# Kernel optimization log

Hardware: AMD Instinct MI355X
Metric: run time of the kernel (lower is better)

The kernel has to match this reference:

```python
import jax, jax.numpy as jnp
import numpy as np

DN = ('NCHW', 'OIHW', 'NCHW')

def _conv(x, w, pad):
    return jax.lax.conv_general_dilated(x, w, window_strides=(1, 1),
                                        padding=[(pad, pad), (pad, pad)],
                                        dimension_numbers=DN)

def _channel_shuffle(x, perm):
    # x: [B, C, H, W]; perm: [C, H*W] per-channel spatial permutation
    B, C, H, W = x.shape
    y = jnp.take_along_axis(x.reshape(B, C, H * W), perm[None, :, :], axis=2)
    return y.reshape(B, C, H, W)

def setup_inputs() -> dict:
    key = jax.random.key(0)
    k = jax.random.split(key, 6)
    B, Cin, H, W = 32, 1024, 28, 28
    P1, P2, P3 = 256, 256, 1024
    HW = H * W
    x = jax.random.normal(k[0], (B, Cin, H, W), dtype=jnp.float32)
    w1 = jax.random.normal(k[1], (P1, Cin, 1, 1), dtype=jnp.float32) * np.sqrt(2.0 / Cin)
    wd = jax.random.normal(k[2], (P2, P1, 3, 3), dtype=jnp.float32) * np.sqrt(2.0 / (P1 * 9))
    w3 = jax.random.normal(k[3], (P3, P2, 1, 1), dtype=jnp.float32) * np.sqrt(2.0 / P2)
    perm_dconv = jax.vmap(lambda kk: jax.random.permutation(kk, HW))(
        jax.random.split(k[4], P1)).astype(jnp.int32)
    perm_res = jax.vmap(lambda kk: jax.random.permutation(kk, HW))(
        jax.random.split(k[5], Cin)).astype(jnp.int32)
    return {"x": x, "w1": w1, "wd": wd, "w3": w3,
            "perm_dconv": perm_dconv, "perm_res": perm_res}

def reference(x, w1, wd, w3, perm_dconv, perm_res):
    # conv1 (1x1) + relu
    y = jax.nn.relu(_conv(x, w1, 0))
    # Dconv_shuffle: per-channel spatial shuffle then 3x3 conv (pad=1), relu
    y = _channel_shuffle(y, perm_dconv)
    y = jax.nn.relu(_conv(y, wd, 1))
    # conv3 (1x1)
    y = _conv(y, w3, 0)
    # residual: per-channel spatially shuffled input, add, relu
    res = _channel_shuffle(x, perm_res)
    return jax.nn.relu(y + res)
```

## Files before the change

### kernel.cpp

```cpp
#include <hip/hip_runtime.h>
#include <hip/hip_bf16.h>

#define BATCH 32
#define CIN   1024
#define HW    784
#define WIMG  28
#define PADW  30
#define PADHW 900
#define P1    256
#define P2    256
#define P3    1024
#define NFLAT (BATCH * HW)

typedef __attribute__((ext_vector_type(8))) short bfrag_t;
typedef __attribute__((ext_vector_type(8))) unsigned short usvec8;
typedef __attribute__((ext_vector_type(4))) unsigned short usvec4;
typedef __attribute__((ext_vector_type(4))) float accvec_t;

static __device__ __forceinline__ unsigned short f2bf(float f) {
    union { __hip_bfloat16 h; unsigned short u; } cv;
    cv.h = __float2bfloat16(f);
    return cv.u;
}
static __device__ __forceinline__ float bf2f(unsigned short u) {
    union { float f; unsigned int i; } cv;
    cv.i = ((unsigned int)u) << 16;
    return cv.f;
}

#define GLDS16(g, l) __builtin_amdgcn_global_load_lds(                      \
        (const __attribute__((address_space(1))) void*)(g),                 \
        (__attribute__((address_space(3))) void*)(l), 16, 0, 0)

#define RAW_BARRIER() do {                         \
        __builtin_amdgcn_sched_barrier(0);         \
        __builtin_amdgcn_s_barrier();              \
        __builtin_amdgcn_sched_barrier(0);         \
    } while (0)
#define WAITCNT_VM(N) do {                                        \
        asm volatile("s_waitcnt vmcnt(" #N ")" ::: "memory");     \
        __builtin_amdgcn_sched_barrier(0);                        \
    } while (0)

__global__ __launch_bounds__(256) void prep_kernel(
        const float* __restrict__ x, unsigned short* __restrict__ xt,
        const float* __restrict__ w1, const float* __restrict__ wd,
        const float* __restrict__ w3, unsigned short* __restrict__ w1b,
        unsigned short* __restrict__ wdb, unsigned short* __restrict__ w3b,
        const int* __restrict__ perm, int* __restrict__ permT,
        unsigned short* __restrict__ y1sp) {
    __shared__ __align__(16) unsigned short T[64 * 72];
    const int bid = blockIdx.x;
    const int t   = threadIdx.x;
    if (bid < 6272) {
        const int c0 = (bid & 15) * 64;
        const int n0 = (bid >> 4) * 64;
        const int f  = t & 15;
        const int cg = t >> 4;
        const int n  = n0 + f * 4;
        const int b  = n / HW, hw = n - b * HW;
        const float* xb = x + ((size_t)b * CIN + c0 + cg * 4) * HW + hw;
        float4 v0 = *(const float4*)&xb[0];
        float4 v1 = *(const float4*)&xb[HW];
        float4 v2 = *(const float4*)&xb[2 * HW];
        float4 v3 = *(const float4*)&xb[3 * HW];
        const float* vr[4] = {(const float*)&v0, (const float*)&v1,
                              (const float*)&v2, (const float*)&v3};
#pragma unroll
        for (int q = 0; q < 4; ++q) {
            usvec4 w;
            w[0] = f2bf(vr[0][q]);
            w[1] = f2bf(vr[1][q]);
            w[2] = f2bf(vr[2][q]);
            w[3] = f2bf(vr[3][q]);
            *(usvec4*)&T[(f * 4 + q) * 72 + cg * 4] = w;
        }
        __syncthreads();
#pragma unroll
        for (int it = 0; it < 2; ++it) {
            int idx  = it * 256 + t;
            int hw_l = idx >> 3, cgo = idx & 7;
            usvec8 w = *(const usvec8*)&T[hw_l * 72 + cgo * 8];
            *(usvec8*)&xt[(size_t)(n0 + hw_l) * CIN + c0 + cgo * 8] = w;
        }
    } else if (bid < 10624) {
        int i = (bid - 6272) * 256 + t;
        if (i < 262144) w1b[i] = f2bf(w1[i]);
        int i2 = i - 262144;
        if (i2 >= 0 && i2 < 262144) w3b[i2] = f2bf(w3[i2]);
        int i3 = i - 524288;
        if (i3 >= 0 && i3 < 589824) {
            int m = i3 / 2304, rem = i3 - m * 2304;
            int k = rem / 9, r = rem - k * 9;
            wdb[((size_t)r * P2 + m) * P1 + k] = f2bf(wd[i3]);
        }
    } else if (bid < 11408) {
        int p = bid - 10624;
        permT[p * P1 + t] = perm[t * HW + p];
    } else {
        int z = bid - 11408;
        usvec8 zv = {0, 0, 0, 0, 0, 0, 0, 0};
        *(usvec8*)&y1sp[((size_t)z * 256 + t) * 8] = zv;
    }
}

__global__ __launch_bounds__(512) void shuffle_pad_kernel(const unsigned short* __restrict__ y1c,
                                                          const int* __restrict__ permT,
                                                          unsigned short* __restrict__ y1sp) {
    __shared__ unsigned short Ly[32 * 800];
    const int b  = blockIdx.x >> 3;
    const int c0 = (blockIdx.x & 7) * 32;
    const int t = threadIdx.x;
#pragma unroll
    for (int it = 0; it < 7; ++it) {
        int chunk = it * 512 + t;
        if (chunk < 3136) {
            int c = chunk / 98, off8 = (chunk - c * 98) * 8;
            usvec8 v = *(const usvec8*)&y1c[((size_t)(b * P1 + c0 + c)) * HW + off8];
            *(usvec8*)&Ly[c * 800 + off8] = v;
        }
    }
    __syncthreads();
    const int pc = t & 31, pi = t >> 5;
    unsigned short* yb = y1sp + (size_t)b * PADHW * P1 + c0 + pc;
#pragma unroll 7
    for (int it = 0; it < 49; ++it) {
        int p = it * 16 + pi;
        int pv = permT[p * P1 + c0 + pc];
        unsigned short val = Ly[pc * 800 + pv];
        int ph = p / WIMG, pw = p - ph * WIMG;
        yb[(size_t)((ph + 1) * PADW + pw + 1) * P1] = val;
    }
}

__global__ __launch_bounds__(256) void conv1_kernel(const unsigned short* __restrict__ xt,
                                                    const unsigned short* __restrict__ w1b,
                                                    unsigned short* __restrict__ y1c) {
    __shared__ __align__(16) unsigned short As[2 * 128 * 64];
    __shared__ __align__(16) unsigned short Bs[2 * 128 * 64];
    const int m0 = blockIdx.x * 128;
    const int n0 = blockIdx.y * 128;
    const int t = threadIdx.x;
    const int lane = t & 63, wave = t >> 6;
    const int l15 = lane & 15, quad = lane >> 4;
    const int wm = wave & 1, wn = wave >> 1;
    const int grow = lane >> 3;
    const int gsw  = ((lane & 7) ^ grow) << 3;
    const unsigned short* Asrc[4];
    const unsigned short* Bsrc[4];
    int ldso[4];
#pragma unroll
    for (int j = 0; j < 4; ++j) {
        int q = wave * 4 + j;
        int row = (q << 3) + grow;
        Asrc[j] = w1b + (size_t)(m0 + row) * CIN + gsw;
        Bsrc[j] = xt + (size_t)(n0 + row) * CIN + gsw;
        ldso[j] = q * 512;
    }
    const int coff0 = ((quad)     ^ (l15 & 7)) << 3;
    const int coff1 = ((quad + 4) ^ (l15 & 7)) << 3;

    accvec_t acc[4][4];
    const accvec_t zero = {0.f, 0.f, 0.f, 0.f};
#pragma unroll
    for (int i = 0; i < 4; ++i)
#pragma unroll
        for (int j = 0; j < 4; ++j) acc[i][j] = zero;

    auto stage = [&](int cur, int k0) {
        unsigned short* Ab = As + cur * 8192;
        unsigned short* Bb = Bs + cur * 8192;
#pragma unroll
        for (int j = 0; j < 4; ++j) {
            GLDS16(Asrc[j] + k0, Ab + ldso[j]);
            GLDS16(Bsrc[j] + k0, Bb + ldso[j]);
        }
    };
    auto compute = [&](int cur) {
        const unsigned short* Ab = As + cur * 8192;
        const unsigned short* Bb = Bs + cur * 8192;
        bfrag_t af[4], bfr[4];
#pragma unroll
        for (int i = 0; i < 4; ++i) {
            af[i]  = *(const bfrag_t*)&Ab[(wm * 64 + i * 16 + l15) * 64 + coff0];
            bfr[i] = *(const bfrag_t*)&Bb[(wn * 64 + i * 16 + l15) * 64 + coff0];
        }
#pragma unroll
        for (int im = 0; im < 4; ++im)
#pragma unroll
            for (int in = 0; in < 4; ++in)
                acc[im][in] = __builtin_amdgcn_mfma_f32_16x16x32_bf16(af[im], bfr[in], acc[im][in], 0, 0, 0);
#pragma unroll
        for (int i = 0; i < 4; ++i) {
            af[i]  = *(const bfrag_t*)&Ab[(wm * 64 + i * 16 + l15) * 64 + coff1];
            bfr[i] = *(const bfrag_t*)&Bb[(wn * 64 + i * 16 + l15) * 64 + coff1];
        }
#pragma unroll
        for (int im = 0; im < 4; ++im)
#pragma unroll
            for (int in = 0; in < 4; ++in)
                acc[im][in] = __builtin_amdgcn_mfma_f32_16x16x32_bf16(af[im], bfr[in], acc[im][in], 0, 0, 0);
    };

    stage(0, 0);
    for (int s = 0; s < 16; s += 2) {
        stage(1, (s + 1) << 6);
        WAITCNT_VM(8);
        RAW_BARRIER();
        compute(0);
        RAW_BARRIER();
        if (s + 2 < 16) { stage(0, (s + 2) << 6); WAITCNT_VM(8); }
        else            { WAITCNT_VM(0); }
        RAW_BARRIER();
        compute(1);
        RAW_BARRIER();
    }
#pragma unroll
    for (int in = 0; in < 4; ++in) {
        const int n = n0 + wn * 64 + in * 16 + l15;
        const int b = n / HW, hw = n - b * HW;
#pragma unroll
        for (int im = 0; im < 4; ++im) {
#pragma unroll
            for (int r = 0; r < 4; ++r) {
                const int m = m0 + wm * 64 + im * 16 + (quad << 2) + r;
                float v = acc[im][in][r];
                v = v > 0.f ? v : 0.f;
                y1c[((size_t)(b * P1 + m)) * HW + hw] = f2bf(v);
            }
        }
    }
}

__global__ __launch_bounds__(256) void dconv_res_kernel(const unsigned short* __restrict__ y1sp,
                                                        const unsigned short* __restrict__ wdb,
                                                        unsigned short* __restrict__ y2t,
                                                        const float* __restrict__ x,
                                                        const int* __restrict__ perm_res,
                                                        unsigned short* __restrict__ res) {
    __shared__ __align__(16) unsigned char SM[65536];
    const int bid = blockIdx.x;
    const int t = threadIdx.x;
    if (bid >= 392) {
        float* Lx = (float*)SM;
        const int g0 = (bid - 392) * 8;
#pragma unroll
        for (int it = 0; it < 7; ++it) {
            int chunk = it * 256 + t;
            if (chunk < 1568) {
                int r = chunk / 196, off = (chunk - r * 196) * 4;
                float4 v = *(const float4*)&x[(size_t)(g0 + r) * HW + off];
                *(float4*)&Lx[r * 788 + off] = v;
            }
        }
        __syncthreads();
        const int q0 = t & 63;
#pragma unroll
        for (int rp = 0; rp < 2; ++rp) {
            int r = rp * 4 + (t >> 6);
            int g = g0 + r;
            int m = g & (CIN - 1);
            const int* pr = perm_res + (size_t)m * HW;
#pragma unroll
            for (int it = 0; it < 13; ++it) {
                int q = it * 64 + q0;
                if (q < HW) {
                    int pv = pr[q];
                    res[(size_t)g * HW + q] = f2bf(Lx[r * 788 + pv]);
                }
            }
        }
        return;
    }
    unsigned short* As = (unsigned short*)SM;
    unsigned short* Bs = (unsigned short*)(SM + 32768);
    const int m0 = (bid & 1) * 128;
    const int n0 = (bid >> 1) * 128;
    const int lane = t & 63, wave = t >> 6;
    const int l15 = lane & 15, quad = lane >> 4;
    const int wm = wave & 1, wn = wave >> 1;
    const int grow = lane >> 3;
    const int gsw  = ((lane & 7) ^ grow) << 3;
    const unsigned short* Asrc[4];
    const unsigned short* Bsrc[4];
    int ldso[4];
#pragma unroll
    for (int j = 0; j < 4; ++j) {
        int q = wave * 4 + j;
        int row = (q << 3) + grow;
        Asrc[j] = wdb + (size_t)(m0 + row) * P1 + gsw;
        int n = n0 + row;
        int b = n / HW, hw = n - b * HW;
        int h = hw / WIMG, w = hw - h * WIMG;
        Bsrc[j] = y1sp + ((size_t)b * PADHW + h * PADW + w) * P1 + gsw;
        ldso[j] = q * 512;
    }
    const int coff0 = ((quad)     ^ (l15 & 7)) << 3;
    const int coff1 = ((quad + 4) ^ (l15 & 7)) << 3;

    accvec_t acc[4][4];
    const accvec_t zero = {0.f, 0.f, 0.f, 0.f};
#pragma unroll
    for (int i = 0; i < 4; ++i)
#pragma unroll
        for (int j = 0; j < 4; ++j) acc[i][j] = zero;

    auto stage = [&](int cur, int s) {
        const int r  = s >> 2;
        const int k0 = (s & 3) << 6;
        const int kh = r / 3, kw = r - kh * 3;
        const size_t aoff = (size_t)r * (P1 * P2) + k0;
        const int    toff = (kh * PADW + kw) * P1 + k0;
        unsigned short* Ab = As + cur * 8192;
        unsigned short* Bb = Bs + cur * 8192;
#pragma unroll
        for (int j = 0; j < 4; ++j) {
            GLDS16(Asrc[j] + aoff, Ab + ldso[j]);
            GLDS16(Bsrc[j] + toff, Bb + ldso[j]);
        }
    };
    auto compute = [&](int cur) {
        const unsigned short* Ab = As + cur * 8192;
        const unsigned short* Bb = Bs + cur * 8192;
        bfrag_t af[4], bfr[4];
#pragma unroll
        for (int i = 0; i < 4; ++i) {
            af[i]  = *(const bfrag_t*)&Ab[(wm * 64 + i * 16 + l15) * 64 + coff0];
            bfr[i] = *(const bfrag_t*)&Bb[(wn * 64 + i * 16 + l15) * 64 + coff0];
        }
#pragma unroll
        for (int im = 0; im < 4; ++im)
#pragma unroll
            for (int in = 0; in < 4; ++in)
                acc[im][in] = __builtin_amdgcn_mfma_f32_16x16x32_bf16(bfr[in], af[im], acc[im][in], 0, 0, 0);
#pragma unroll
        for (int i = 0; i < 4; ++i) {
            af[i]  = *(const bfrag_t*)&Ab[(wm * 64 + i * 16 + l15) * 64 + coff1];
            bfr[i] = *(const bfrag_t*)&Bb[(wn * 64 + i * 16 + l15) * 64 + coff1];
        }
#pragma unroll
        for (int im = 0; im < 4; ++im)
#pragma unroll
            for (int in = 0; in < 4; ++in)
                acc[im][in] = __builtin_amdgcn_mfma_f32_16x16x32_bf16(bfr[in], af[im], acc[im][in], 0, 0, 0);
    };

    stage(0, 0);
    for (int s = 0; s < 36; s += 2) {
        stage(1, s + 1);
        WAITCNT_VM(8);
        RAW_BARRIER();
        compute(0);
        RAW_BARRIER();
        if (s + 2 < 36) { stage(0, s + 2); WAITCNT_VM(8); }
        else            { WAITCNT_VM(0); }
        RAW_BARRIER();
        compute(1);
        RAW_BARRIER();
    }
#pragma unroll
    for (int im = 0; im < 4; ++im) {
        const int m = m0 + wm * 64 + im * 16 + l15;
#pragma unroll
        for (int in = 0; in < 4; ++in) {
#pragma unroll
            for (int r = 0; r < 4; ++r) {
                const int n = n0 + wn * 64 + in * 16 + (quad << 2) + r;
                float v = acc[im][in][r];
                v = v > 0.f ? v : 0.f;
                y2t[(size_t)n * P2 + m] = f2bf(v);
            }
        }
    }
}

__global__ __launch_bounds__(256) void conv3_kernel(const unsigned short* __restrict__ y2t,
                                                    const unsigned short* __restrict__ w3b,
                                                    const unsigned short* __restrict__ res,
                                                    float* __restrict__ out) {
    __shared__ __align__(16) unsigned short SMEM[16384];
    unsigned short* AsB = SMEM;
    unsigned short* BsB = SMEM + 8192;
    float* Obuf = (float*)SMEM;

    const int m0 = blockIdx.x * 128;
    const int n0 = blockIdx.y * 128;
    const int t = threadIdx.x;
    const int lane = t & 63, wave = t >> 6;
    const int l15 = lane & 15, quad = lane >> 4;
    const int wm = wave & 1, wn = wave >> 1;
    const int srow = lane >> 2, c8 = (lane & 3) << 3;
    const int row0 = wave * 32 + srow, row1 = row0 + 16;

    const unsigned short* a0 = w3b + (size_t)(m0 + row0) * P2 + c8;
    const unsigned short* a1 = w3b + (size_t)(m0 + row1) * P2 + c8;
    const unsigned short* b0 = y2t + (size_t)(n0 + row0) * P2 + c8;
    const unsigned short* b1 = y2t + (size_t)(n0 + row1) * P2 + c8;
    const int o0 = (wave * 2 + 0) * 512, o1 = (wave * 2 + 1) * 512;

    const int erow = t >> 3, eseg = t & 7;
    const int n_e  = n0 + eseg * 16;
    const int b_e  = n_e / HW;
    const int hw_e = n_e - b_e * HW;
    const size_t ebase0 = ((size_t)(b_e * P3 + m0 + erow)) * HW + hw_e;

    usvec8 rsA = *(const usvec8*)&res[ebase0];
    usvec8 rsB = *(const usvec8*)&res[ebase0 + 8];

    accvec_t acc[4][4];
    const accvec_t zero = {0.f, 0.f, 0.f, 0.f};
#pragma unroll
    for (int i = 0; i < 4; ++i)
#pragma unroll
        for (int j = 0; j < 4; ++j) acc[i][j] = zero;

    auto stage = [&](int cur, int k0) {
        unsigned short* Ab = AsB + cur * 4096;
        unsigned short* Bb = BsB + cur * 4096;
        GLDS16(a0 + k0, Ab + o0);
        GLDS16(a1 + k0, Ab + o1);
        GLDS16(b0 + k0, Bb + o0);
        GLDS16(b1 + k0, Bb + o1);
    };
    auto compute = [&](int cur) {
        const unsigned short* Ab = AsB + cur * 4096;
        const unsigned short* Bb = BsB + cur * 4096;
        bfrag_t af[4], bfr[4];
#pragma unroll
        for (int i = 0; i < 4; ++i) {
            af[i]  = *(const bfrag_t*)&Ab[(wm * 64 + i * 16 + l15) * 32 + (quad << 3)];
            bfr[i] = *(const bfrag_t*)&Bb[(wn * 64 + i * 16 + l15) * 32 + (quad << 3)];
        }
#pragma unroll
        for (int im = 0; im < 4; ++im)
#pragma unroll
            for (int in = 0; in < 4; ++in)
                acc[im][in] = __builtin_amdgcn_mfma_f32_16x16x32_bf16(af[im], bfr[in], acc[im][in], 0, 0, 0);
    };

    stage(0, 0);
    for (int s = 0; s < 8; s += 2) {
        stage(1, (s + 1) << 5);
        WAITCNT_VM(4);
        RAW_BARRIER();
        compute(0);
        RAW_BARRIER();
        if (s + 2 < 8) { stage(0, (s + 2) << 5); WAITCNT_VM(4); }
        else           { WAITCNT_VM(0); }
        RAW_BARRIER();
        compute(1);
        RAW_BARRIER();
    }

#pragma unroll
    for (int c = 0; c < 4; ++c) {
        if (wm == (c >> 1)) {
            const int imb = (c & 1) * 2;
#pragma unroll
            for (int i2 = 0; i2 < 2; ++i2)
#pragma unroll
                for (int in = 0; in < 4; ++in)
#pragma unroll
                    for (int r = 0; r < 4; ++r)
                        Obuf[(i2 * 16 + (quad << 2) + r) * 132 + wn * 64 + in * 16 + l15] =
                            acc[imb + i2][in][r];
        }
        __syncthreads();
        usvec8 nxA = rsA, nxB = rsB;
        if (c < 3) {
            const size_t nb = ebase0 + (size_t)(c + 1) * 32 * HW;
            nxA = *(const usvec8*)&res[nb];
            nxB = *(const usvec8*)&res[nb + 8];
        }
        {
            const size_t base = ebase0 + (size_t)c * 32 * HW;
            float ov[16];
#pragma unroll
            for (int q4 = 0; q4 < 4; ++q4) {
                float4 v = *(const float4*)&Obuf[erow * 132 + eseg * 16 + q4 * 4];
                ov[q4 * 4 + 0] = v.x; ov[q4 * 4 + 1] = v.y;
                ov[q4 * 4 + 2] = v.z; ov[q4 * 4 + 3] = v.w;
            }
#pragma unroll
            for (int q4 = 0; q4 < 4; ++q4) {
                float4 w;
                float e0, e1, e2, e3;
                const int j = q4 * 4;
                e0 = ov[j + 0] + bf2f((unsigned short)(j + 0 < 8 ? rsA[j + 0] : rsB[j + 0 - 8]));
                e1 = ov[j + 1] + bf2f((unsigned short)(j + 1 < 8 ? rsA[j + 1] : rsB[j + 1 - 8]));
                e2 = ov[j + 2] + bf2f((unsigned short)(j + 2 < 8 ? rsA[j + 2] : rsB[j + 2 - 8]));
                e3 = ov[j + 3] + bf2f((unsigned short)(j + 3 < 8 ? rsA[j + 3] : rsB[j + 3 - 8]));
                w.x = e0 > 0.f ? e0 : 0.f;
                w.y = e1 > 0.f ? e1 : 0.f;
                w.z = e2 > 0.f ? e2 : 0.f;
                w.w = e3 > 0.f ? e3 : 0.f;
                *(float4*)&out[base + q4 * 4] = w;
            }
        }
        rsA = nxA; rsB = nxB;
        if (c < 3) __syncthreads();
    }
}

extern "C" void kernel_launch(void* const* d_in, const int* in_sizes, int n_in,
                              void* d_out, int out_size, void* d_ws, size_t ws_size,
                              hipStream_t stream) {
    const float* x      = (const float*)d_in[0];
    const float* w1     = (const float*)d_in[1];
    const float* wd     = (const float*)d_in[2];
    const float* w3     = (const float*)d_in[3];
    const int*   perm_d = (const int*)d_in[4];
    const int*   perm_r = (const int*)d_in[5];
    float*       out    = (float*)d_out;

    char* ws = (char*)d_ws;
    unsigned short* y1sp  = (unsigned short*)(ws + 0);
    unsigned short* y2t   = (unsigned short*)(ws + 14745600);
    int*            permT = (int*)(ws + 27590656);
    unsigned short* w1b   = (unsigned short*)(ws + 28393472);
    unsigned short* wdb   = (unsigned short*)(ws + 28917760);
    unsigned short* w3b   = (unsigned short*)(ws + 30097408);
    unsigned short* xt    = (unsigned short*)(ws + 30621696);
    unsigned short* resb  = xt;
    unsigned short* y1c   = y2t;

    prep_kernel<<<dim3(15008), dim3(256), 0, stream>>>(x, xt, w1, wd, w3,
                                                       w1b, wdb, w3b,
                                                       perm_d, permT, y1sp);
    conv1_kernel<<<dim3(P1 / 128, NFLAT / 128), dim3(256), 0, stream>>>(xt, w1b, y1c);
    shuffle_pad_kernel<<<dim3(BATCH * 8), dim3(512), 0, stream>>>(y1c, permT, y1sp);
    dconv_res_kernel<<<dim3(392 + BATCH * CIN / 8), dim3(256), 0, stream>>>(
        y1sp, wdb, y2t, x, perm_r, resb);
    conv3_kernel<<<dim3(P3 / 128, NFLAT / 128), dim3(256), 0, stream>>>(y2t, w3b, resb, out);
}
```

Baseline: 331.5 us.

## Remap GEMM block order for XCD-local L2 reuse and move aux work into conv1

Block indices for conv1, dconv and conv3 are now remapped so each group of blocks sharing bid mod 8 (likely the same XCD under round-robin dispatch) works on a contiguous range of output tiles. Tiles that share the same activation rows then stay within one L2. The permutation transpose and the zeroing of the padded buffer move from the prep kernel into extra blocks of the conv1 launch, so they run alongside GEMM tiles instead of lengthening prep. The remapping assumes the hardware dispatches blocks to XCDs round-robin, and the extra blocks add branch overhead to the conv1 kernel.

```diff
diff --git a/kernel.cpp b/kernel.cpp
--- a/kernel.cpp
+++ b/kernel.cpp
@@ -46,9 +46,7 @@
         const float* __restrict__ x, unsigned short* __restrict__ xt,
         const float* __restrict__ w1, const float* __restrict__ wd,
         const float* __restrict__ w3, unsigned short* __restrict__ w1b,
-        unsigned short* __restrict__ wdb, unsigned short* __restrict__ w3b,
-        const int* __restrict__ perm, int* __restrict__ permT,
-        unsigned short* __restrict__ y1sp) {
+        unsigned short* __restrict__ wdb, unsigned short* __restrict__ w3b) {
     __shared__ __align__(16) unsigned short T[64 * 72];
     const int bid = blockIdx.x;
     const int t   = threadIdx.x;
@@ -83,7 +81,7 @@
             usvec8 w = *(const usvec8*)&T[hw_l * 72 + cgo * 8];
             *(usvec8*)&xt[(size_t)(n0 + hw_l) * CIN + c0 + cgo * 8] = w;
         }
-    } else if (bid < 10624) {
+    } else {
         int i = (bid - 6272) * 256 + t;
         if (i < 262144) w1b[i] = f2bf(w1[i]);
         int i2 = i - 262144;
@@ -94,13 +92,6 @@
             int k = rem / 9, r = rem - k * 9;
             wdb[((size_t)r * P2 + m) * P1 + k] = f2bf(wd[i3]);
         }
-    } else if (bid < 11408) {
-        int p = bid - 10624;
-        permT[p * P1 + t] = perm[t * HW + p];
-    } else {
-        int z = bid - 11408;
-        usvec8 zv = {0, 0, 0, 0, 0, 0, 0, 0};
-        *(usvec8*)&y1sp[((size_t)z * 256 + t) * 8] = zv;
     }
 }
 
@@ -133,14 +124,29 @@
     }
 }
 
-__global__ __launch_bounds__(256) void conv1_kernel(const unsigned short* __restrict__ xt,
-                                                    const unsigned short* __restrict__ w1b,
-                                                    unsigned short* __restrict__ y1c) {
+__global__ __launch_bounds__(256) void conv1_aux_kernel(
+        const unsigned short* __restrict__ xt, const unsigned short* __restrict__ w1b,
+        unsigned short* __restrict__ y1c,
+        const int* __restrict__ perm, int* __restrict__ permT,
+        unsigned short* __restrict__ y1sp) {
     __shared__ __align__(16) unsigned short As[2 * 128 * 64];
     __shared__ __align__(16) unsigned short Bs[2 * 128 * 64];
-    const int m0 = blockIdx.x * 128;
-    const int n0 = blockIdx.y * 128;
+    const int bid = blockIdx.x;
     const int t = threadIdx.x;
+    if (bid >= 1176) {
+        int z = bid - 1176;
+        usvec8 zv = {0, 0, 0, 0, 0, 0, 0, 0};
+        *(usvec8*)&y1sp[((size_t)z * 256 + t) * 8] = zv;
+        return;
+    }
+    if (bid >= 392) {
+        int p = bid - 392;
+        permT[p * P1 + t] = perm[t * HW + p];
+        return;
+    }
+    const int l = (bid & 7) * 49 + (bid >> 3);
+    const int m0 = (l & 1) * 128;
+    const int n0 = (l >> 1) * 128;
     const int lane = t & 63, wave = t >> 6;
     const int l15 = lane & 15, quad = lane >> 4;
     const int wm = wave & 1, wn = wave >> 1;
@@ -274,8 +280,9 @@
     }
     unsigned short* As = (unsigned short*)SM;
     unsigned short* Bs = (unsigned short*)(SM + 32768);
-    const int m0 = (bid & 1) * 128;
-    const int n0 = (bid >> 1) * 128;
+    const int l = (bid & 7) * 49 + (bid >> 3);
+    const int m0 = (l & 1) * 128;
+    const int n0 = (l >> 1) * 128;
     const int lane = t & 63, wave = t >> 6;
     const int l15 = lane & 15, quad = lane >> 4;
     const int wm = wave & 1, wn = wave >> 1;
@@ -383,8 +390,10 @@
     unsigned short* BsB = SMEM + 8192;
     float* Obuf = (float*)SMEM;
 
-    const int m0 = blockIdx.x * 128;
-    const int n0 = blockIdx.y * 128;
+    const int bid = blockIdx.x;
+    const int l  = (bid & 7) * 196 + (bid >> 3);
+    const int m0 = (l & 7) * 128;
+    const int n0 = (l >> 3) * 128;
     const int t = threadIdx.x;
     const int lane = t & 63, wave = t >> 6;
     const int l15 = lane & 15, quad = lane >> 4;
@@ -524,12 +533,12 @@
     unsigned short* resb  = xt;
     unsigned short* y1c   = y2t;
 
-    prep_kernel<<<dim3(15008), dim3(256), 0, stream>>>(x, xt, w1, wd, w3,
-                                                       w1b, wdb, w3b,
-                                                       perm_d, permT, y1sp);
-    conv1_kernel<<<dim3(P1 / 128, NFLAT / 128), dim3(256), 0, stream>>>(xt, w1b, y1c);
+    prep_kernel<<<dim3(10624), dim3(256), 0, stream>>>(x, xt, w1, wd, w3,
+                                                       w1b, wdb, w3b);
+    conv1_aux_kernel<<<dim3(4776), dim3(256), 0, stream>>>(xt, w1b, y1c,
+                                                           perm_d, permT, y1sp);
     shuffle_pad_kernel<<<dim3(BATCH * 8), dim3(512), 0, stream>>>(y1c, permT, y1sp);
     dconv_res_kernel<<<dim3(392 + BATCH * CIN / 8), dim3(256), 0, stream>>>(
         y1sp, wdb, y2t, x, perm_r, resb);
-    conv3_kernel<<<dim3(P3 / 128, NFLAT / 128), dim3(256), 0, stream>>>(y2t, w3b, resb, out);
-}
+    conv3_kernel<<<dim3(1568), dim3(256), 0, stream>>>(y2t, w3b, resb, out);
+}
```

Result: no change. 329.0 us (-0.7%).
